# Kernel tuning notes

Measured on AMD Instinct MI355X. Metric: run time of the kernel, lower is better.

The kernel has to match this reference:

```python
import jax, jax.numpy as jnp
import numpy as np

IOU_THRESHOLD = 0.5

def cxcywh_to_xyxy(b):
    cx, cy, w, h = jnp.split(b, 4, axis=-1)
    return jnp.concatenate([cx - 0.5 * w, cy - 0.5 * h, cx + 0.5 * w, cy + 0.5 * h], axis=-1)

def batched_giou(p_xyxy, t_xyxy):
    # p_xyxy: [B, N, 4], t_xyxy: [B, T, 4] -> giou: [B, N, T]
    p = p_xyxy[:, :, None, :]  # [B, N, 1, 4]
    t = t_xyxy[:, None, :, :]  # [B, 1, T, 4]
    area_p = (p_xyxy[..., 2] - p_xyxy[..., 0]) * (p_xyxy[..., 3] - p_xyxy[..., 1])  # [B, N]
    area_t = (t_xyxy[..., 2] - t_xyxy[..., 0]) * (t_xyxy[..., 3] - t_xyxy[..., 1])  # [B, T]
    lt = jnp.maximum(p[..., :2], t[..., :2])
    rb = jnp.minimum(p[..., 2:], t[..., 2:])
    wh = jnp.clip(rb - lt, 0.0)
    inter = wh[..., 0] * wh[..., 1]  # [B, N, T]
    union = area_p[:, :, None] + area_t[:, None, :] - inter
    iou = inter / union
    # enclosing box
    lt_e = jnp.minimum(p[..., :2], t[..., :2])
    rb_e = jnp.maximum(p[..., 2:], t[..., 2:])
    wh_e = jnp.clip(rb_e - lt_e, 0.0)
    area_e = wh_e[..., 0] * wh_e[..., 1]
    return iou - (area_e - union) / area_e

def setup_inputs() -> dict:
    key = jax.random.key(0)
    k1, k2 = jax.random.split(key)
    B, N, T = 128, 900, 300
    pred_boxes = jax.random.uniform(k1, (B, N, 4), dtype=jnp.float32)
    target_boxes = jax.random.uniform(k2, (B, T, 4), dtype=jnp.float32)
    target_mask = jnp.ones((B, T), dtype=bool)
    return {"pred_boxes": pred_boxes, "target_boxes": target_boxes, "target_mask": target_mask}

def reference(pred_boxes, target_boxes, target_mask):
    # pred_boxes: [B, N, 4] cxcywh; target_boxes: [B, T, 4] cxcywh (padded)
    p_xyxy = cxcywh_to_xyxy(pred_boxes)
    t_xyxy = cxcywh_to_xyxy(target_boxes)
    giou = batched_giou(p_xyxy, t_xyxy)  # [B, N, T]
    max_iou = jnp.max(giou, axis=1)      # [B, T] best GIoU per target
    pred_idx = jnp.argmax(giou, axis=1)  # [B, T] matched query per target
    valid = target_mask & (max_iou >= IOU_THRESHOLD)  # [B, T] match kept
    return pred_idx, valid, max_iou
```

## Files before the change

### kernel.cpp

```cpp
#include <hip/hip_runtime.h>


#define BB 128
#define NN 900
#define TT 300
#define TCHUNK 64
#define TBLOCKS 5
#define NSPLIT 5
#define NPB 180
#define NPW 45
#define MARGIN 1e-5f

__device__ __forceinline__ float fdiv_fast(float n, float d) {
    float r = __builtin_amdgcn_rcpf(d);
    float q = n * r;
    float e = fmaf(-d, q, n);
    return fmaf(e, r, q);
}

__device__ __forceinline__ float giou_exact(float4 pb, float4 tb) {
#pragma clang fp contract(off)
    float px0 = pb.x - 0.5f * pb.z, py0 = pb.y - 0.5f * pb.w;
    float px1 = pb.x + 0.5f * pb.z, py1 = pb.y + 0.5f * pb.w;
    float tx0 = tb.x - 0.5f * tb.z, ty0 = tb.y - 0.5f * tb.w;
    float tx1 = tb.x + 0.5f * tb.z, ty1 = tb.y + 0.5f * tb.w;
    float pa = (px1 - px0) * (py1 - py0);
    float ta = (tx1 - tx0) * (ty1 - ty0);
    float w  = fmaxf(fminf(px1, tx1) - fmaxf(px0, tx0), 0.f);
    float h  = fmaxf(fminf(py1, ty1) - fmaxf(py0, ty0), 0.f);
    float inter = w * h;
    float uni   = pa + ta - inter;
    float iou   = inter / uni;
    float ew = fmaxf(fmaxf(px1, tx1) - fminf(px0, tx0), 0.f);
    float eh = fmaxf(fmaxf(py1, ty1) - fminf(py0, ty0), 0.f);
    float ea = ew * eh;
    return iou - (ea - uni) / ea;
}

__global__ __launch_bounds__(256) void matcher_scan_kernel(
    const float* __restrict__ pred,
    const float* __restrict__ tgt,
    float* __restrict__ pbest,
    float* __restrict__ psec,
    int*   __restrict__ pidx)
{
    __shared__ float4 sp[NPB];
    __shared__ float  spa[NPB];
    __shared__ float  rbv[256], rsv[256];
    __shared__ int    riv[256];

    const int ns  = blockIdx.x % NSPLIT;
    const int tc  = (blockIdx.x / NSPLIT) % TBLOCKS;
    const int b   = blockIdx.x / (NSPLIT * TBLOCKS);
    const int tid = threadIdx.x;
    const int tl  = tid & 63;
    const int ng  = tid >> 6;
    const int t   = tc * TCHUNK + tl;

    if (tid < NPB) {
        const float4 pb = ((const float4*)pred)[b * NN + ns * NPB + tid];
        float4 q;
        q.x = pb.x - 0.5f * pb.z;
        q.y = pb.y - 0.5f * pb.w;
        q.z = pb.x + 0.5f * pb.z;
        q.w = pb.y + 0.5f * pb.w;
        sp[tid]  = q;
        spa[tid] = (q.z - q.x) * (q.w - q.y);
    }
    __syncthreads();

    float tx0 = 0.f, ty0 = 0.f, tx1 = 0.f, ty1 = 0.f, ta = 0.f;
    if (t < TT) {
        const float4 tb = ((const float4*)tgt)[b * TT + t];
        tx0 = tb.x - 0.5f * tb.z;
        ty0 = tb.y - 0.5f * tb.w;
        tx1 = tb.x + 0.5f * tb.z;
        ty1 = tb.y + 0.5f * tb.w;
        ta  = (tx1 - tx0) * (ty1 - ty0);
    }

    float best = -INFINITY, second = -INFINITY;
    int   bidx = 0;
    const int k0 = ng * NPW;
    #pragma unroll 5
    for (int k = 0; k < NPW; ++k) {
        const float4 p = sp[k0 + k];
        const float pa = spa[k0 + k];

        const float w   = fmaxf(fminf(p.z, tx1) - fmaxf(p.x, tx0), 0.f);
        const float h   = fmaxf(fminf(p.w, ty1) - fmaxf(p.y, ty0), 0.f);
        const float inter = w * h;
        const float uni   = pa + ta - inter;
        const float iou   = fdiv_fast(inter, uni);

        const float ew = fmaxf(fmaxf(p.z, tx1) - fminf(p.x, tx0), 0.f);
        const float eh = fmaxf(fmaxf(p.w, ty1) - fminf(p.y, ty0), 0.f);
        const float ea = ew * eh;
        const float g  = iou - fdiv_fast(ea - uni, ea);

        second = __builtin_amdgcn_fmed3f(g, best, second);
        if (g > best) { bidx = k0 + k; }
        best = fmaxf(best, g);
    }

    rbv[tid] = best; rsv[tid] = second; riv[tid] = bidx;
    __syncthreads();

    if (ng == 0 && t < TT) {
        for (int s = 1; s < 4; ++s) {
            const float ob = rbv[s * 64 + tl];
            const float os = rsv[s * 64 + tl];
            const int   oi = riv[s * 64 + tl];
            second = fmaxf(fminf(best, ob), fmaxf(second, os));
            if (ob > best) { best = ob; bidx = oi; }
        }
        const int bt = b * TT + t;
        pbest[ns * BB * TT + bt] = best;
        psec [ns * BB * TT + bt] = second;
        pidx [ns * BB * TT + bt] = ns * NPB + bidx;
    }
}

__global__ __launch_bounds__(256) void matcher_combine_kernel(
    const float* __restrict__ pbest,
    const float* __restrict__ psec,
    const int*   __restrict__ pidx,
    const float* __restrict__ pred,
    const float* __restrict__ tgt,
    const unsigned char* __restrict__ mask,
    float* __restrict__ out,
    int*   __restrict__ counter,
    int*   __restrict__ flagged)
{
    const int bt = blockIdx.x * 256 + threadIdx.x;
    if (bt >= BB * TT) return;

    float best = -INFINITY, second = -INFINITY;
    int   bidx = 0;
    for (int s = 0; s < NSPLIT; ++s) {
        const float ob = pbest[s * BB * TT + bt];
        const float os = psec [s * BB * TT + bt];
        const int   oi = pidx [s * BB * TT + bt];
        second = fmaxf(fminf(best, ob), fmaxf(second, os));
        if (ob > best) { best = ob; bidx = oi; }
    }

    if (best - second > MARGIN) {
        const int b = bt / TT;
        const float4 pb = ((const float4*)pred)[b * NN + bidx];
        const float4 tb = ((const float4*)tgt)[bt];
        const float g = giou_exact(pb, tb);
        const bool valid = (mask[bt] != 0) && (g >= 0.5f);
        out[bt]               = (float)bidx;
        out[BB * TT + bt]     = valid ? 1.f : 0.f;
        out[2 * BB * TT + bt] = g;
    } else {
        const int pos = atomicAdd(counter, 1);
        flagged[pos] = bt;
    }
}

__global__ __launch_bounds__(256) void matcher_rescan_kernel(
    const float* __restrict__ pred,
    const float* __restrict__ tgt,
    const unsigned char* __restrict__ mask,
    const int*   __restrict__ counter,
    const int*   __restrict__ flagged,
    float* __restrict__ out)
{
    const int wave   = (blockIdx.x * 256 + threadIdx.x) >> 6;
    const int lane   = threadIdx.x & 63;
    const int nwaves = gridDim.x * 4;
    const int cnt    = *counter;

    for (int f = wave; f < cnt; f += nwaves) {
        const int bt = flagged[f];
        const int b  = bt / TT;
        const float4 tb = ((const float4*)tgt)[bt];

        float best = -INFINITY;
        int   bidx = NN;
        for (int n = lane; n < NN; n += 64) {
            const float4 pb = ((const float4*)pred)[b * NN + n];
            const float g = giou_exact(pb, tb);
            if (g > best) { best = g; bidx = n; }
        }
        for (int off = 32; off >= 1; off >>= 1) {
            const float ob = __shfl_xor(best, off);
            const int   oi = __shfl_xor(bidx, off);
            if (ob > best || (ob == best && oi < bidx)) { best = ob; bidx = oi; }
        }
        if (lane == 0) {
            const bool valid = (mask[bt] != 0) && (best >= 0.5f);
            out[bt]               = (float)bidx;
            out[BB * TT + bt]     = valid ? 1.f : 0.f;
            out[2 * BB * TT + bt] = best;
        }
    }
}

extern "C" void kernel_launch(void* const* d_in, const int* in_sizes, int n_in,
                              void* d_out, int out_size, void* d_ws, size_t ws_size,
                              hipStream_t stream) {
    const float* pred = (const float*)d_in[0];
    const float* tgt  = (const float*)d_in[1];
    const unsigned char* mask = (const unsigned char*)d_in[2];
    float* out = (float*)d_out;

    char* ws = (char*)d_ws;
    int*   counter = (int*)ws;
    int*   flagged = (int*)(ws + 64);
    float* pbest   = (float*)(ws + 64 + BB * TT * 4);
    float* psec    = (float*)(ws + 64 + BB * TT * 4 * 6);
    int*   pidx    = (int*)  (ws + 64 + BB * TT * 4 * 11);

    hipMemsetAsync(counter, 0, sizeof(int), stream);
    matcher_scan_kernel<<<dim3(BB * TBLOCKS * NSPLIT), dim3(256), 0, stream>>>(
        pred, tgt, pbest, psec, pidx);
    matcher_combine_kernel<<<dim3((BB * TT + 255) / 256), dim3(256), 0, stream>>>(
        pbest, psec, pidx, pred, tgt, mask, out, counter, flagged);
    matcher_rescan_kernel<<<dim3(64), dim3(256), 0, stream>>>(
        pred, tgt, mask, counter, flagged, out);
}
```

Measured before the change: 107.7 us.

## Merge combine and rescan kernels, use one reciprocal per GIoU, finer N split

The scan loop now computes GIoU as a single fused numerator times one hardware reciprocal of uni*ea, replacing two Newton-refined divisions. The margin widens to absorb the larger approximation error. The N dimension is split 9 ways instead of 5 for more blocks. The combine and rescan kernels are merged: ambiguous targets are queued in shared memory and rescanned exactly inside the same block, which removes the memset, the global atomic counter and one launch. The trade-off is more partial results to reduce and possible block-level imbalance when a block has many flagged targets.

```diff
diff --git a/kernel.cpp b/kernel.cpp
--- a/kernel.cpp
+++ b/kernel.cpp
@@ -6,17 +6,10 @@
 #define TT 300
 #define TCHUNK 64
 #define TBLOCKS 5
-#define NSPLIT 5
-#define NPB 180
-#define NPW 45
-#define MARGIN 1e-5f
-
-__device__ __forceinline__ float fdiv_fast(float n, float d) {
-    float r = __builtin_amdgcn_rcpf(d);
-    float q = n * r;
-    float e = fmaf(-d, q, n);
-    return fmaf(e, r, q);
-}
+#define NSPLIT 9
+#define NPB 100
+#define NPW 25
+#define MARGIN 2e-5f
 
 __device__ __forceinline__ float giou_exact(float4 pb, float4 tb) {
 #pragma clang fp contract(off)
@@ -91,12 +84,13 @@
         const float h   = fmaxf(fminf(p.w, ty1) - fmaxf(p.y, ty0), 0.f);
         const float inter = w * h;
         const float uni   = pa + ta - inter;
-        const float iou   = fdiv_fast(inter, uni);
-
-        const float ew = fmaxf(fmaxf(p.z, tx1) - fminf(p.x, tx0), 0.f);
-        const float eh = fmaxf(fmaxf(p.w, ty1) - fminf(p.y, ty0), 0.f);
+
+        const float ew = fmaxf(p.z, tx1) - fminf(p.x, tx0);
+        const float eh = fmaxf(p.w, ty1) - fminf(p.y, ty0);
         const float ea = ew * eh;
-        const float g  = iou - fdiv_fast(ea - uni, ea);
+
+        const float num = fmaf(inter, ea, uni * (uni - ea));
+        const float g   = num * __builtin_amdgcn_rcpf(uni * ea);
 
         second = __builtin_amdgcn_fmed3f(g, best, second);
         if (g > best) { bidx = k0 + k; }
@@ -121,19 +115,22 @@
     }
 }
 
-__global__ __launch_bounds__(256) void matcher_combine_kernel(
+__global__ __launch_bounds__(256) void matcher_finish_kernel(
     const float* __restrict__ pbest,
     const float* __restrict__ psec,
     const int*   __restrict__ pidx,
     const float* __restrict__ pred,
     const float* __restrict__ tgt,
     const unsigned char* __restrict__ mask,
-    float* __restrict__ out,
-    int*   __restrict__ counter,
-    int*   __restrict__ flagged)
+    float* __restrict__ out)
 {
-    const int bt = blockIdx.x * 256 + threadIdx.x;
-    if (bt >= BB * TT) return;
+    __shared__ int sflag[256];
+    __shared__ int scount;
+
+    const int tid = threadIdx.x;
+    const int bt  = blockIdx.x * 256 + tid;
+    if (tid == 0) scount = 0;
+    __syncthreads();
 
     float best = -INFINITY, second = -INFINITY;
     int   bidx = 0;
@@ -155,46 +152,36 @@
         out[BB * TT + bt]     = valid ? 1.f : 0.f;
         out[2 * BB * TT + bt] = g;
     } else {
-        const int pos = atomicAdd(counter, 1);
-        flagged[pos] = bt;
-    }
-}
-
-__global__ __launch_bounds__(256) void matcher_rescan_kernel(
-    const float* __restrict__ pred,
-    const float* __restrict__ tgt,
-    const unsigned char* __restrict__ mask,
-    const int*   __restrict__ counter,
-    const int*   __restrict__ flagged,
-    float* __restrict__ out)
-{
-    const int wave   = (blockIdx.x * 256 + threadIdx.x) >> 6;
-    const int lane   = threadIdx.x & 63;
-    const int nwaves = gridDim.x * 4;
-    const int cnt    = *counter;
-
-    for (int f = wave; f < cnt; f += nwaves) {
-        const int bt = flagged[f];
-        const int b  = bt / TT;
-        const float4 tb = ((const float4*)tgt)[bt];
-
-        float best = -INFINITY;
-        int   bidx = NN;
+        const int pos = atomicAdd(&scount, 1);
+        sflag[pos] = tid;
+    }
+    __syncthreads();
+
+    const int cnt  = scount;
+    const int lane = tid & 63;
+    const int ng   = tid >> 6;
+    for (int f = ng; f < cnt; f += 4) {
+        const int fbt = blockIdx.x * 256 + sflag[f];
+        const int b   = fbt / TT;
+        const float4 tb = ((const float4*)tgt)[fbt];
+
+        float bestx = -INFINITY;
+        int   bix   = NN;
         for (int n = lane; n < NN; n += 64) {
             const float4 pb = ((const float4*)pred)[b * NN + n];
             const float g = giou_exact(pb, tb);
-            if (g > best) { best = g; bidx = n; }
+            if (g > bestx) { bestx = g; bix = n; }
         }
         for (int off = 32; off >= 1; off >>= 1) {
-            const float ob = __shfl_xor(best, off);
-            const int   oi = __shfl_xor(bidx, off);
-            if (ob > best || (ob == best && oi < bidx)) { best = ob; bidx = oi; }
+            const float ob = __shfl_xor(bestx, off);
+            const int   oi = __shfl_xor(bix, off);
+            if (ob > bestx || (ob == bestx && oi < bix)) { bestx = ob; bix = oi; }
         }
         if (lane == 0) {
-            const bool valid = (mask[bt] != 0) && (best >= 0.5f);
-            out[bt]               = (float)bidx;
-            out[BB * TT + bt]     = valid ? 1.f : 0.f;
-            out[2 * BB * TT + bt] = best;
+            const bool valid = (mask[fbt] != 0) && (bestx >= 0.5f);
+            out[fbt]               = (float)bix;
+            out[BB * TT + fbt]     = valid ? 1.f : 0.f;
+            out[2 * BB * TT + fbt] = bestx;
         }
     }
 }
@@ -207,18 +194,14 @@
     const unsigned char* mask = (const unsigned char*)d_in[2];
     float* out = (float*)d_out;
 
+    const size_t seg = (size_t)NSPLIT * BB * TT * 4;
     char* ws = (char*)d_ws;
-    int*   counter = (int*)ws;
-    int*   flagged = (int*)(ws + 64);
-    float* pbest   = (float*)(ws + 64 + BB * TT * 4);
-    float* psec    = (float*)(ws + 64 + BB * TT * 4 * 6);
-    int*   pidx    = (int*)  (ws + 64 + BB * TT * 4 * 11);
-
-    hipMemsetAsync(counter, 0, sizeof(int), stream);
+    float* pbest = (float*)ws;
+    float* psec  = (float*)(ws + seg);
+    int*   pidx  = (int*)  (ws + 2 * seg);
+
     matcher_scan_kernel<<<dim3(BB * TBLOCKS * NSPLIT), dim3(256), 0, stream>>>(
         pred, tgt, pbest, psec, pidx);
-    matcher_combine_kernel<<<dim3((BB * TT + 255) / 256), dim3(256), 0, stream>>>(
-        pbest, psec, pidx, pred, tgt, mask, out, counter, flagged);
-    matcher_rescan_kernel<<<dim3(64), dim3(256), 0, stream>>>(
-        pred, tgt, mask, counter, flagged, out);
-}
+    matcher_finish_kernel<<<dim3(BB * TT / 256), dim3(256), 0, stream>>>(
+        pbest, psec, pidx, pred, tgt, mask, out);
+}
```

Measured after the change: 95.58 us. 1.13x faster.
